# Kernel optimization log

Measured on AMD Instinct MI355X. Metric: run time of the kernel, lower is better.

## Reference

```python
import jax, jax.numpy as jnp
import numpy as np


def spiral_cw(H, W):
    idx = []
    top, bottom, left, right = 0, H - 1, 0, W - 1
    while top <= bottom and left <= right:
        for j in range(left, right + 1):
            idx.append((top, j))
        top += 1
        for i in range(top, bottom + 1):
            idx.append((i, right))
        right -= 1
        if top <= bottom:
            for j in range(right, left - 1, -1):
                idx.append((bottom, j))
            bottom -= 1
        if left <= right:
            for i in range(bottom, top - 1, -1):
                idx.append((i, left))
            left += 1
    return [i * W + j for i, j in idx]


def spiral_ccw(H, W):
    idx = []
    top, bottom, left, right = 0, H - 1, 0, W - 1
    while top <= bottom and left <= right:
        for j in range(right, left - 1, -1):
            idx.append((top, j))
        top += 1
        for i in range(top, bottom + 1):
            idx.append((i, left))
        left += 1
        if top <= bottom:
            for j in range(left, right + 1):
                idx.append((bottom, j))
            bottom -= 1
        if left <= right:
            for i in range(bottom, top - 1, -1):
                idx.append((i, right))
            right -= 1
    return [i * W + j for i, j in idx]


def silu(x):
    return x * jax.nn.sigmoid(x)


def mamba_fwd(x, in_w, conv_w, conv_b, xproj_w, dtp_w, dtp_b, A_log, D, out_w):
    # x: [B,L,dm]; expand=1 so d_inner == dm
    B, L, dm = x.shape
    d_inner = in_w.shape[1] // 2
    N = A_log.shape[1]          # d_state = 16
    K = conv_w.shape[1]         # d_conv = 4
    xz = x @ in_w               # [B,L,2*d_inner]
    u, z = jnp.split(xz, 2, axis=-1)
    # causal depthwise conv over L (kernel K), then SiLU
    up = jnp.pad(u, ((0, 0), (K - 1, 0), (0, 0)))
    uc = conv_b + sum(conv_w[:, k] * up[:, k:k + L, :] for k in range(K))
    uc = silu(uc)
    dbl = uc @ xproj_w          # [B,L,dt_rank+2N]
    dt_rank = dbl.shape[-1] - 2 * N
    dtc = dbl[..., :dt_rank]
    Bv = dbl[..., dt_rank:dt_rank + N]
    Cv = dbl[..., dt_rank + N:]
    dt = jax.nn.softplus(dtc @ dtp_w + dtp_b)   # [B,L,d_inner]
    A = -jnp.exp(A_log)                          # [d_inner,N]
    dA = jnp.exp(dt[..., None] * A)              # [B,L,d_inner,N]
    dBu = dt[..., None] * Bv[:, :, None, :] * uc[..., None]

    def step(h, inp):
        dA_t, dBu_t = inp
        h = h * dA_t + dBu_t
        return h, h

    h0 = jnp.zeros((B, d_inner, N), x.dtype)
    _, hs = jax.lax.scan(step, h0, (jnp.moveaxis(dA, 1, 0), jnp.moveaxis(dBu, 1, 0)))
    hs = jnp.moveaxis(hs, 0, 1)                  # [B,L,d_inner,N]
    y = jnp.einsum('bldn,bln->bld', hs, Cv) + D * uc
    y = y * silu(z)
    return y @ out_w


def setup_inputs():
    key = jax.random.key(0)
    ks = jax.random.split(key, 32)
    B, Hh, Ww, C = 4, 32, 32, 768
    L = Hh * Ww
    N, dr, K = 16, 48, 4

    def p(i, shape, s=0.02):
        return jax.random.normal(ks[i], shape, jnp.float32) * s

    d = {}
    d['x'] = jax.random.normal(ks[0], (B, L, C), jnp.float32)
    d['norm_w'] = jnp.ones((C,), jnp.float32)
    d['norm_b'] = jnp.zeros((C,), jnp.float32)
    for i, pre in enumerate(['cw', 'ccw']):
        o = 1 + i * 8
        d[pre + '_in_w'] = p(o, (C, 2 * C))
        d[pre + '_conv_w'] = p(o + 1, (C, K), 0.2)
        d[pre + '_conv_b'] = jnp.zeros((C,), jnp.float32)
        d[pre + '_xproj_w'] = p(o + 2, (C, dr + 2 * N))
        d[pre + '_dtp_w'] = p(o + 3, (dr, C), 0.1)
        d[pre + '_dtp_b'] = jnp.full((C,), -4.0, jnp.float32) + p(o + 4, (C,), 0.5)
        d[pre + '_A_log'] = jnp.log(jnp.broadcast_to(jnp.arange(1, N + 1, dtype=jnp.float32), (C, N)))
        d[pre + '_D'] = jnp.ones((C,), jnp.float32)
        d[pre + '_out_w'] = p(o + 5, (C, C))
    d['fus_w1'] = p(20, (2 * C, C))
    d['fus_b1'] = jnp.zeros((C,), jnp.float32)
    d['fus_w2'] = p(21, (C, C))
    d['fus_b2'] = jnp.zeros((C,), jnp.float32)
    return d


def reference(x, norm_w, norm_b,
              cw_in_w, cw_conv_w, cw_conv_b, cw_xproj_w, cw_dtp_w, cw_dtp_b, cw_A_log, cw_D, cw_out_w,
              ccw_in_w, ccw_conv_w, ccw_conv_b, ccw_xproj_w, ccw_dtp_w, ccw_dtp_b, ccw_A_log, ccw_D, ccw_out_w,
              fus_w1, fus_b1, fus_w2, fus_b2):
    B, L, C = x.shape
    H = int(L ** 0.5)
    W = H
    idx_cw = jnp.asarray(np.array(spiral_cw(H, W), dtype=np.int32))
    idx_ccw = jnp.asarray(np.array(spiral_ccw(H, W), dtype=np.int32))
    rev_cw = jnp.argsort(idx_cw)
    rev_ccw = jnp.argsort(idx_ccw)
    # LayerNorm(eps=1e-6)
    mu = x.mean(-1, keepdims=True)
    var = x.var(-1, keepdims=True)
    xn = (x - mu) / jnp.sqrt(var + 1e-6) * norm_w + norm_b
    x_cw = mamba_fwd(xn[:, idx_cw, :], cw_in_w, cw_conv_w, cw_conv_b, cw_xproj_w,
                     cw_dtp_w, cw_dtp_b, cw_A_log, cw_D, cw_out_w)[:, rev_cw, :]
    x_ccw = mamba_fwd(xn[:, idx_ccw, :], ccw_in_w, ccw_conv_w, ccw_conv_b, ccw_xproj_w,
                      ccw_dtp_w, ccw_dtp_b, ccw_A_log, ccw_D, ccw_out_w)[:, rev_ccw, :]
    fused = jnp.concatenate([x_cw, x_ccw], axis=-1)
    h = jax.nn.gelu(fused @ fus_w1 + fus_b1, approximate=False)
    out = h @ fus_w2 + fus_b2
    return out + x
```

## Files before the change

kernel.cpp:

```cpp
#include <hip/hip_runtime.h>

typedef unsigned short ushort_t;
typedef __attribute__((ext_vector_type(8))) short short8;
typedef __attribute__((ext_vector_type(4))) float f32x4;
typedef __attribute__((ext_vector_type(4))) unsigned short u16x4;

#define B_ 4
#define L_ 1024
#define C_ 768
#define N_ 16
#define DR_ 48
#define HW_ 32
#define M_ (B_*L_)
#define SEG_ 64
#define NSEG_ 16


__device__ __forceinline__ float bf2f(ushort_t u) {
  union { unsigned int i; float f; } v; v.i = ((unsigned int)u) << 16; return v.f;
}
__device__ __forceinline__ ushort_t f2bf(float f) {
  union { float f; unsigned int i; } v; v.f = f;
  unsigned int x = v.i;
  return (ushort_t)((x + 0x7fffu + ((x >> 16) & 1u)) >> 16);
}
__device__ __forceinline__ float ldf(const void* p, size_t i, int bf) {
  return bf ? bf2f(((const ushort_t*)p)[i]) : ((const float*)p)[i];
}
__device__ __forceinline__ int detect_bf(const void* x) {
  const ushort_t* u = (const ushort_t*)x;
  int lane = threadIdx.x & 63;
  const ushort_t* p = u + lane * 4;
  int bad = 0;
  #pragma unroll
  for (int i = 0; i < 4; ++i) {
    int e = (p[i] >> 7) & 0xFF;
    bad |= (e < 90 || e > 141);
  }
  return (__ballot(bad) == 0ull) ? 1 : 0;
}
__device__ __forceinline__ void gload_lds16(const void* g, void* lds) {
  __builtin_amdgcn_global_load_lds(
      (const __attribute__((address_space(1))) unsigned int*)g,
      (__attribute__((address_space(3))) unsigned int*)lds, 16, 0, 0);
}

struct TJ {
  const void* src[8]; ushort_t* dst[8];
  int R[8], Cc[8], RD[8], ldD[8];
  int off[9]; int njobs;
};

__global__ __launch_bounds__(256) void prep_k(
    TJ tj, const void* __restrict__ x, const void* __restrict__ nw,
    const void* __restrict__ nb, ushort_t* __restrict__ xn,
    int* idx_cw, int* idx_ccw, int* flag)
{
  const int oT = tj.off[tj.njobs];
  int bid = blockIdx.x;
  const int inbf = detect_bf(x);

  if (bid < oT) {
    int j = 0;
    while (bid >= tj.off[j+1]) ++j;
    const void* src = tj.src[j];
    ushort_t* dst = tj.dst[j];
    const int R = tj.R[j], Cc = tj.Cc[j], RD = tj.RD[j], ldD = tj.ldD[j];
    int cb_span = (Cc > RD ? Cc : RD);
    int txt = (cb_span + 31) >> 5;
    int t = bid - tj.off[j];
    int bx = (t % txt) * 32;
    int by = (t / txt) * 32;
    __shared__ ushort_t tile[32][33];
    int tx = threadIdx.x & 31, ty = threadIdx.x >> 5;
    #pragma unroll
    for (int i = 0; i < 4; ++i) {
      int r = by + ty + i*8, c = bx + tx;
      ushort_t v = 0;
      if (r < R && c < Cc) v = f2bf(ldf(src, (size_t)r * Cc + c, inbf));
      tile[ty + i*8][tx] = v;
    }
    __syncthreads();
    #pragma unroll
    for (int i = 0; i < 4; ++i) {
      int dr = bx + ty + i*8, dc = by + tx;
      if (dr < RD && dc < ldD)
        dst[(size_t)dr * ldD + dc] = tile[tx][ty + i*8];
    }
    return;
  }
  bid -= oT;
  if (bid < M_) {
    int tid = threadIdx.x;
    size_t o0 = (size_t)bid * C_;
    float v0 = ldf(x, o0 + tid,       inbf);
    float v1 = ldf(x, o0 + tid + 256, inbf);
    float v2 = ldf(x, o0 + tid + 512, inbf);
    float s = v0 + v1 + v2, s2 = v0*v0 + v1*v1 + v2*v2;
    for (int o = 32; o > 0; o >>= 1) { s += __shfl_down(s, o); s2 += __shfl_down(s2, o); }
    __shared__ float ss[4], ss2[4];
    if ((tid & 63) == 0) { ss[tid >> 6] = s; ss2[tid >> 6] = s2; }
    __syncthreads();
    s  = ss[0] + ss[1] + ss[2] + ss[3];
    s2 = ss2[0] + ss2[1] + ss2[2] + ss2[3];
    float mean = s * (1.f / C_);
    float var  = s2 * (1.f / C_) - mean * mean;
    float inv  = rsqrtf(var + 1e-6f);
    xn[o0 + tid]       = f2bf((v0 - mean) * inv * ldf(nw, tid,     inbf) + ldf(nb, tid,     inbf));
    xn[o0 + tid + 256] = f2bf((v1 - mean) * inv * ldf(nw, tid+256, inbf) + ldf(nb, tid+256, inbf));
    xn[o0 + tid + 512] = f2bf((v2 - mean) * inv * ldf(nw, tid+512, inbf) + ldf(nb, tid+512, inbf));
    return;
  }
  {
    int tid = threadIdx.x;
    #pragma unroll
    for (int k = 0; k < 4; ++k) {
      int p = tid * 4 + k;
      int r = 0;
      while (r < (HW_/2 - 1) && p >= 4*(r+1)*(HW_-(r+1))) ++r;
      int q = p - 4*r*(HW_-r);
      int s = HW_ - 2*r;
      int hi = HW_ - 1 - r;
      int icw, jcw, iccw, jccw;
      if (q < s)              { icw = r;                  jcw = r + q; }
      else if (q < 2*s-1)     { icw = r + 1 + (q - s);    jcw = hi; }
      else if (q < 3*s-2)     { icw = hi;                 jcw = hi - 1 - (q - (2*s-1)); }
      else                    { icw = hi - 1 - (q - (3*s-2)); jcw = r; }
      if (q < s)              { iccw = r;                 jccw = hi - q; }
      else if (q < 2*s-1)     { iccw = r + 1 + (q - s);   jccw = r; }
      else if (q < 3*s-2)     { iccw = hi;                jccw = r + 1 + (q - (2*s-1)); }
      else                    { iccw = hi - 1 - (q - (3*s-2)); jccw = hi; }
      idx_cw[p]  = icw  * HW_ + jcw;
      idx_ccw[p] = iccw * HW_ + jccw;
    }
    if (tid == 0) *flag = inbf;
  }
}

__global__ __launch_bounds__(256) void tbatch_k(TJ tj, const int* __restrict__ flagp) {
  const int inbf = *flagp;
  int bid = blockIdx.x;
  int j = 0;
  while (bid >= tj.off[j+1]) ++j;
  const void* src = tj.src[j];
  ushort_t* dst = tj.dst[j];
  const int R = tj.R[j], Cc = tj.Cc[j], RD = tj.RD[j], ldD = tj.ldD[j];
  int cb_span = (Cc > RD ? Cc : RD);
  int txt = (cb_span + 31) >> 5;
  int t = bid - tj.off[j];
  int bx = (t % txt) * 32;
  int by = (t / txt) * 32;
  __shared__ ushort_t tile[32][33];
  int tx = threadIdx.x & 31, ty = threadIdx.x >> 5;
  #pragma unroll
  for (int i = 0; i < 4; ++i) {
    int r = by + ty + i*8, c = bx + tx;
    ushort_t v = 0;
    if (r < R && c < Cc) v = f2bf(ldf(src, (size_t)r * Cc + c, inbf));
    tile[ty + i*8][tx] = v;
  }
  __syncthreads();
  #pragma unroll
  for (int i = 0; i < 4; ++i) {
    int dr = bx + ty + i*8, dc = by + tx;
    if (dr < RD && dc < ldD)
      dst[(size_t)dr * ldD + dc] = tile[tx][ty + i*8];
  }
}

struct GB {
  const ushort_t* A[4]; const int* amap[4];
  const ushort_t* WT[4];
  const void* bias[4];
  void* out[4]; ushort_t* out2[4]; const int* omap[4];
};

template<int BM, int BN>
__global__ __launch_bounds__(256) void mgemm_k(
    GB gb, int lda, int ldb, int Nn, int K, int ldo,
    int act, int out_mode, const void* resid, int ldr, const int* __restrict__ flagp)
{
  constexpr int NA = BM / 32;
  constexpr int NB = BN / 32;
  constexpr int WN = (BM == 128) ? 2 : 4;
  constexpr int NSPAN = BN / WN;
  constexpr int FN = NSPAN / 16;
  const int inbf = *flagp;
  const int z = blockIdx.z;

  const ushort_t* A  = gb.A[z];
  const int* amap    = gb.amap[z];
  const ushort_t* Bw = gb.WT[z];
  const void* bias   = gb.bias[z];
  void* Out          = gb.out[z];
  ushort_t* out2     = gb.out2[z];
  const int* omap    = gb.omap[z];

  __shared__ __align__(16) ushort_t As[BM * 64];
  __shared__ __align__(16) ushort_t Bs[BN * 64];

  const int tid  = threadIdx.x;
  const int w    = tid >> 6;
  const int lane = tid & 63;
  const int quad = lane >> 4;
  const int l15  = lane & 15;
  const int wm     = (BM == 128) ? (w >> 1) * 64 : 0;
  const int wn_off = ((BM == 128) ? (w & 1) : w) * NSPAN;
  const int row0 = blockIdx.y * BM;
  const int col0 = blockIdx.x * BN;

  int agb[NA], bgb[NB], aldso[NA], bldso[NB];
  #pragma unroll
  for (int i = 0; i < NA; ++i) {
    int t = i*256 + tid;
    int r = t >> 3;
    int c = (t & 7) ^ (r & 7);
    int grow = row0 + r;
    if (amap) { int b = grow >> 10, l = grow & 1023; grow = (b << 10) + amap[l]; }
    agb[i] = grow * lda + c * 8;
    aldso[i] = (i*256 + w*64) * 16;
  }
  #pragma unroll
  for (int i = 0; i < NB; ++i) {
    int t = i*256 + tid;
    int r = t >> 3;
    int c = (t & 7) ^ (r & 7);
    bgb[i] = (col0 + r) * ldb + c * 8;
    bldso[i] = (i*256 + w*64) * 16;
  }

  f32x4 acc[4][FN];
  #pragma unroll
  for (int mi = 0; mi < 4; ++mi)
    #pragma unroll
    for (int ni = 0; ni < FN; ++ni)
      acc[mi][ni] = (f32x4){0.f, 0.f, 0.f, 0.f};

  const int sw = l15 & 7;

  for (int k0 = 0; k0 < K; k0 += 64) {
    #pragma unroll
    for (int i = 0; i < NA; ++i)
      gload_lds16(A + agb[i] + k0, (char*)As + aldso[i]);
    #pragma unroll
    for (int i = 0; i < NB; ++i)
      gload_lds16(Bw + bgb[i] + k0, (char*)Bs + bldso[i]);
    __syncthreads();

    #pragma unroll
    for (int ks = 0; ks < 2; ++ks) {
      short8 aF[4], bF[FN];
      #pragma unroll
      for (int mi = 0; mi < 4; ++mi)
        aF[mi] = *(const short8*)&As[(wm + mi*16 + l15) * 64 + (((quad + 4*ks) ^ sw) * 8)];
      #pragma unroll
      for (int ni = 0; ni < FN; ++ni)
        bF[ni] = *(const short8*)&Bs[(wn_off + ni*16 + l15) * 64 + (((quad + 4*ks) ^ sw) * 8)];
      #pragma unroll
      for (int mi = 0; mi < 4; ++mi)
        #pragma unroll
        for (int ni = 0; ni < FN; ++ni)
          acc[mi][ni] = __builtin_amdgcn_mfma_f32_16x16x32_bf16(aF[mi], bF[ni], acc[mi][ni], 0, 0, 0);
    }
    __syncthreads();
  }

  const int obf = (out_mode == 2) ? inbf : (out_mode == 0);
  #pragma unroll
  for (int ni = 0; ni < FN; ++ni) {
    int colg = col0 + wn_off + ni*16 + l15;
    if (colg >= Nn) continue;
    float bv = bias ? ldf(bias, colg, inbf) : 0.f;
    #pragma unroll
    for (int mi = 0; mi < 4; ++mi) {
      #pragma unroll
      for (int r = 0; r < 4; ++r) {
        int rowg = row0 + wm + mi*16 + quad*4 + r;
        int orow = rowg;
        if (omap) { int b = rowg >> 10, l = rowg & 1023; orow = (b << 10) + omap[l]; }
        float v = acc[mi][ni][r] + bv;
        if (out2 && colg < 64)
          out2[(size_t)orow * 64 + colg] = f2bf(colg < DR_ ? v : 0.f);
        if (act == 1)      v = (v > 20.f) ? v : log1pf(__expf(v));
        else if (act == 2) v = 0.5f * v * (1.f + erff(v * 0.70710678118654752f));
        if (resid) v += ldf(resid, (size_t)orow * ldr + colg, inbf);
        size_t oi = (size_t)orow * ldo + colg;
        if (obf) ((ushort_t*)Out)[oi] = f2bf(v);
        else     ((float*)Out)[oi]    = v;
      }
    }
  }
}

__global__ __launch_bounds__(256) void conv_silu_k(
    const ushort_t* __restrict__ u,
    const void* __restrict__ cw0, const void* __restrict__ cw1,
    const void* __restrict__ cb0, const void* __restrict__ cb1,
    ushort_t* __restrict__ uc, const int* __restrict__ flagp)
{
  const int inbf = *flagp;
  int g = blockIdx.x * 256 + threadIdx.x;
  int c = g % C_;
  int row = g / C_;
  int l = row & 1023;
  const void* cw = (row >> 12) ? cw1 : cw0;
  const void* cb = (row >> 12) ? cb1 : cb0;
  float w0 = ldf(cw, c*4+0, inbf), w1 = ldf(cw, c*4+1, inbf);
  float w2 = ldf(cw, c*4+2, inbf), w3 = ldf(cw, c*4+3, inbf);
  const ushort_t* up = u + (size_t)(row - l) * C_ + c;
  float s = ldf(cb, c, inbf);
  if (l >= 3) s += w0 * bf2f(up[(size_t)(l-3) * C_]);
  if (l >= 2) s += w1 * bf2f(up[(size_t)(l-2) * C_]);
  if (l >= 1) s += w2 * bf2f(up[(size_t)(l-1) * C_]);
  s += w3 * bf2f(up[(size_t)l * C_]);
  s = s / (1.f + __expf(-s));
  uc[g] = f2bf(s);
}

__global__ __launch_bounds__(256) void scan_pass1(
    const ushort_t* __restrict__ dt, const ushort_t* __restrict__ uc,
    const float* __restrict__ dbl,
    const void* __restrict__ Alog_cw, const void* __restrict__ Alog_ccw,
    ushort_t* __restrict__ P, ushort_t* __restrict__ Q,
    const int* __restrict__ flagp)
{
  const int inbf = *flagp;
  const int db = blockIdx.z, d = db >> 2;
  const int s = blockIdx.y;
  const int tid = threadIdx.x;
  const int cl = tid >> 2;
  const int n4 = tid & 3;
  const int c = blockIdx.x * 64 + cl;
  const int l0 = s * SEG_;

  __shared__ __align__(16) float Bs[SEG_][32];
  {
    const float* src = dbl + ((size_t)db * L_ + l0) * 80 + DR_;
    #pragma unroll
    for (int i = 0; i < 2; ++i) {
      int idx = tid * 4 + i * 1024;
      int st = idx >> 5, col = idx & 31;
      *(f32x4*)&Bs[st][col] = *(const f32x4*)(src + (size_t)st * 80 + col);
    }
  }
  __syncthreads();

  const void* Alog = d ? Alog_ccw : Alog_cw;
  float a[4];
  #pragma unroll
  for (int j = 0; j < 4; ++j) a[j] = -__expf(ldf(Alog, c * N_ + n4*4 + j, inbf));

  const size_t rbase = ((size_t)db * L_ + l0) * C_ + c;
  const ushort_t* dtp = dt + rbase;
  const ushort_t* ucp = uc + rbase;

  float h[4] = {0.f, 0.f, 0.f, 0.f};
  float S = 0.f;

  #pragma unroll 8
  for (int l = 0; l < SEG_; ++l) {
    float dtv = bf2f(dtp[(size_t)l * C_]);
    float ucv = bf2f(ucp[(size_t)l * C_]);
    float dtu = dtv * ucv;
    S += dtv;
    f32x4 bq = *(const f32x4*)&Bs[l][n4*4];
    #pragma unroll
    for (int j = 0; j < 4; ++j) { float dA = __expf(dtv*a[j]); h[j] = h[j]*dA + dtu*bq[j]; }
  }
  size_t idx = (((size_t)db * NSEG_ + s) * C_ + c) * N_ + n4*4;
  u16x4 pv, qv;
  #pragma unroll
  for (int j = 0; j < 4; ++j) { pv[j] = f2bf(__expf(a[j] * S)); qv[j] = f2bf(h[j]); }
  *(u16x4*)&P[idx] = pv;
  *(u16x4*)&Q[idx] = qv;
}

__global__ __launch_bounds__(256) void scan_pass2(
    ushort_t* __restrict__ P, ushort_t* __restrict__ Q)
{
  size_t g = (size_t)blockIdx.x * 256 + threadIdx.x;
  size_t db = g / (C_ * N_);
  size_t cn = g % (C_ * N_);
  float h = 0.f;
  #pragma unroll
  for (int s = 0; s < NSEG_; ++s) {
    size_t off = (db * NSEG_ + s) * (C_ * N_) + cn;
    float p = bf2f(P[off]), q = bf2f(Q[off]);
    Q[off] = f2bf(h);
    h = h * p + q;
  }
}

__global__ __launch_bounds__(256) void scan_pass3(
    const ushort_t* __restrict__ dt, const ushort_t* __restrict__ uc,
    const float* __restrict__ dbl, const ushort_t* __restrict__ z,
    const void* __restrict__ Alog_cw, const void* __restrict__ Alog_ccw,
    const void* __restrict__ D_cw, const void* __restrict__ D_ccw,
    const ushort_t* __restrict__ Q, ushort_t* __restrict__ y,
    const int* __restrict__ flagp)
{
  const int inbf = *flagp;
  const int db = blockIdx.z, d = db >> 2;
  const int s = blockIdx.y;
  const int tid = threadIdx.x;
  const int cl = tid >> 2;
  const int n4 = tid & 3;
  const int c = blockIdx.x * 64 + cl;
  const int l0 = s * SEG_;

  __shared__ __align__(16) float Bs[SEG_][32];
  {
    const float* src = dbl + ((size_t)db * L_ + l0) * 80 + DR_;
    #pragma unroll
    for (int i = 0; i < 2; ++i) {
      int idx = tid * 4 + i * 1024;
      int st = idx >> 5, col = idx & 31;
      *(f32x4*)&Bs[st][col] = *(const f32x4*)(src + (size_t)st * 80 + col);
    }
  }
  __syncthreads();

  const void* Alog = d ? Alog_ccw : Alog_cw;
  const void* Dp   = d ? D_ccw   : D_cw;
  float a[4];
  #pragma unroll
  for (int j = 0; j < 4; ++j) a[j] = -__expf(ldf(Alog, c * N_ + n4*4 + j, inbf));
  const float dvc = ldf(Dp, c, inbf);

  const size_t rbase = ((size_t)db * L_ + l0) * C_ + c;
  const ushort_t* dtp = dt + rbase;
  const ushort_t* ucp = uc + rbase;
  const ushort_t* zp  = z  + rbase;
  ushort_t* yp = y + rbase;

  size_t idx = (((size_t)db * NSEG_ + s) * C_ + c) * N_ + n4*4;
  float h[4];
  #pragma unroll
  for (int j = 0; j < 4; ++j) h[j] = bf2f(Q[idx + j]);

  #pragma unroll 4
  for (int l = 0; l < SEG_; ++l) {
    float dtv = bf2f(dtp[(size_t)l * C_]);
    float ucv = bf2f(ucp[(size_t)l * C_]);
    float zv  = bf2f(zp[(size_t)l * C_]);
    float dtu = dtv * ucv;
    f32x4 bq = *(const f32x4*)&Bs[l][n4*4];
    f32x4 cq = *(const f32x4*)&Bs[l][16 + n4*4];
    float yv = 0.f;
    #pragma unroll
    for (int j = 0; j < 4; ++j) { float dA = __expf(dtv*a[j]); h[j] = h[j]*dA + dtu*bq[j]; yv += h[j]*cq[j]; }
    yv += __shfl_xor(yv, 1);
    yv += __shfl_xor(yv, 2);
    if (n4 == 0) {
      float o = yv + dvc * ucv;
      o *= zv / (1.f + __expf(-zv));
      yp[(size_t)l * C_] = f2bf(o);
    }
  }
}

extern "C" void kernel_launch(void* const* d_in, const int* in_sizes, int n_in,
                              void* d_out, int out_size, void* d_ws, size_t ws_size,
                              hipStream_t stream)
{
  const void* x      = d_in[0];
  const void* norm_w = d_in[1];
  const void* norm_b = d_in[2];
  const void* in_w[2]    = { d_in[3],  d_in[12] };
  const void* conv_w[2]  = { d_in[4],  d_in[13] };
  const void* conv_b[2]  = { d_in[5],  d_in[14] };
  const void* xproj_w[2] = { d_in[6],  d_in[15] };
  const void* dtp_w[2]   = { d_in[7],  d_in[16] };
  const void* dtp_b[2]   = { d_in[8],  d_in[17] };
  const void* A_log[2]   = { d_in[9],  d_in[18] };
  const void* Dvec[2]    = { d_in[10], d_in[19] };
  const void* out_w[2]   = { d_in[11], d_in[20] };
  const void* fus_w1 = d_in[21];
  const void* fus_b1 = d_in[22];
  const void* fus_w2 = d_in[23];
  const void* fus_b2 = d_in[24];

  char* base = (char*)d_ws;
  int*      IDX  = (int*)base;
  int*      FLAG = (int*)(base + 8192);
  ushort_t* XN   = (ushort_t*)(base + 8448);
  ushort_t* U    = (ushort_t*)(base + 6299904);
  ushort_t* Z    = (ushort_t*)(base + 18882816);
  ushort_t* UC   = (ushort_t*)(base + 31465728);
  float*    DBL  = (float*)(base + 44048640);
  ushort_t* Y    = (ushort_t*)(base + 46670080);
  ushort_t* DT    = U;
  ushort_t* FUSED = Z;
  ushort_t* HBUF  = XN;
  ushort_t* SP = (ushort_t*)(base + 8448);
  ushort_t* SQ = SP + (size_t)2 * 4 * NSEG_ * C_ * N_;
  ushort_t* DTC = XN;
  ushort_t* INWT = UC;
  ushort_t* uout = (ushort_t*)d_out;
  ushort_t* XPJT = uout;
  ushort_t* DTPT = uout + 196608;
  ushort_t* OWT  = uout + 294912;
  ushort_t* FW1T = U;
  ushort_t* FW2T = U + (size_t)768 * 1536;

  const size_t SD = (size_t)M_ * C_;

  {
    TJ tj; tj.njobs = 8;
    for (int d = 0; d < 2; ++d) {
      int j = d;
      tj.src[j]=in_w[d]; tj.dst[j]=INWT+(size_t)d*1536*768;
      tj.R[j]=768; tj.Cc[j]=1536; tj.RD[j]=1536; tj.ldD[j]=768;
    }
    for (int d = 0; d < 2; ++d) {
      int j = 2+d;
      tj.src[j]=xproj_w[d]; tj.dst[j]=XPJT+(size_t)d*128*768;
      tj.R[j]=768; tj.Cc[j]=80; tj.RD[j]=128; tj.ldD[j]=768;
    }
    for (int d = 0; d < 2; ++d) {
      int j = 4+d;
      tj.src[j]=dtp_w[d]; tj.dst[j]=DTPT+(size_t)d*768*64;
      tj.R[j]=48; tj.Cc[j]=768; tj.RD[j]=768; tj.ldD[j]=64;
    }
    for (int d = 0; d < 2; ++d) {
      int j = 6+d;
      tj.src[j]=out_w[d]; tj.dst[j]=OWT+(size_t)d*768*768;
      tj.R[j]=768; tj.Cc[j]=768; tj.RD[j]=768; tj.ldD[j]=768;
    }
    tj.off[0] = 0;
    for (int j = 0; j < 8; ++j) {
      int cspan = tj.Cc[j] > tj.RD[j] ? tj.Cc[j] : tj.RD[j];
      int rspan = tj.R[j] > tj.ldD[j] ? tj.R[j] : tj.ldD[j];
      tj.off[j+1] = tj.off[j] + ((cspan+31)>>5) * ((rspan+31)>>5);
    }
    int nblk = tj.off[8] + M_ + 1;
    hipLaunchKernelGGL(prep_k, dim3(nblk), dim3(256), 0, stream,
        tj, x, norm_w, norm_b, XN, IDX, IDX + L_, FLAG);
  }

  GB gb;
  for (int i = 0; i < 4; ++i) { gb.out2[i] = nullptr; gb.omap[i] = nullptr; gb.amap[i] = nullptr; gb.bias[i] = nullptr; }

  for (int zz = 0; zz < 4; ++zz) {
    int d = zz >> 1, half = zz & 1;
    gb.A[zz] = XN; gb.amap[zz] = IDX + d * L_;
    gb.WT[zz] = INWT + (size_t)d*1536*768 + (size_t)half*768*768;
    gb.bias[zz] = nullptr;
    gb.out[zz] = (void*)((half ? Z : U) + d * SD); gb.out2[zz] = nullptr; gb.omap[zz] = nullptr;
  }
  hipLaunchKernelGGL((mgemm_k<64,64>), dim3(12, 64, 4), dim3(256), 0, stream,
      gb, C_, C_, C_, C_, C_, 0, 0, (const void*)nullptr, 0, FLAG);

  hipLaunchKernelGGL(conv_silu_k, dim3(2*M_*C_/256), dim3(256), 0, stream,
      U, conv_w[0], conv_w[1], conv_b[0], conv_b[1], UC, FLAG);

  for (int zz = 0; zz < 2; ++zz) {
    gb.A[zz] = UC + zz * SD; gb.amap[zz] = nullptr;
    gb.WT[zz] = XPJT + (size_t)zz*128*768;
    gb.bias[zz] = nullptr;
    gb.out[zz] = (void*)(DBL + (size_t)zz * M_ * 80);
    gb.out2[zz] = DTC + (size_t)zz * M_ * 64;
    gb.omap[zz] = nullptr;
  }
  hipLaunchKernelGGL((mgemm_k<64,64>), dim3(2, 64, 2), dim3(256), 0, stream,
      gb, C_, C_, 80, C_, 80, 0, 1, (const void*)nullptr, 0, FLAG);

  for (int zz = 0; zz < 2; ++zz) {
    gb.A[zz] = DTC + (size_t)zz * M_ * 64; gb.amap[zz] = nullptr;
    gb.WT[zz] = DTPT + (size_t)zz*768*64;
    gb.bias[zz] = dtp_b[zz];
    gb.out[zz] = (void*)(DT + zz * SD); gb.out2[zz] = nullptr; gb.omap[zz] = nullptr;
  }
  hipLaunchKernelGGL((mgemm_k<64,64>), dim3(12, 64, 2), dim3(256), 0, stream,
      gb, 64, 64, C_, 64, C_, 1, 0, (const void*)nullptr, 0, FLAG);

  hipLaunchKernelGGL(scan_pass1, dim3(12, NSEG_, 8), dim3(256), 0, stream,
      DT, UC, DBL, A_log[0], A_log[1], SP, SQ, FLAG);
  hipLaunchKernelGGL(scan_pass2, dim3(8 * C_ * N_ / 256), dim3(256), 0, stream, SP, SQ);
  hipLaunchKernelGGL(scan_pass3, dim3(12, NSEG_, 8), dim3(256), 0, stream,
      DT, UC, DBL, Z, A_log[0], A_log[1], Dvec[0], Dvec[1], SQ, Y, FLAG);

  {
    TJ tj; tj.njobs = 2;
    tj.src[0]=fus_w1; tj.dst[0]=FW1T; tj.R[0]=1536; tj.Cc[0]=768; tj.RD[0]=768; tj.ldD[0]=1536;
    tj.src[1]=fus_w2; tj.dst[1]=FW2T; tj.R[1]=768;  tj.Cc[1]=768; tj.RD[1]=768; tj.ldD[1]=768;
    tj.off[0] = 0;
    for (int j = 0; j < 2; ++j) {
      int cspan = tj.Cc[j] > tj.RD[j] ? tj.Cc[j] : tj.RD[j];
      int rspan = tj.R[j] > tj.ldD[j] ? tj.R[j] : tj.ldD[j];
      tj.off[j+1] = tj.off[j] + ((cspan+31)>>5) * ((rspan+31)>>5);
    }
    hipLaunchKernelGGL(tbatch_k, dim3(tj.off[2]), dim3(256), 0, stream, tj, FLAG);
  }

  for (int zz = 0; zz < 2; ++zz) {
    gb.A[zz] = Y + zz * SD; gb.amap[zz] = nullptr;
    gb.WT[zz] = OWT + (size_t)zz*768*768;
    gb.bias[zz] = nullptr;
    gb.out[zz] = (void*)(FUSED + zz * C_); gb.out2[zz] = nullptr; gb.omap[zz] = IDX + zz * L_;
  }
  hipLaunchKernelGGL((mgemm_k<64,64>), dim3(12, 64, 2), dim3(256), 0, stream,
      gb, C_, C_, C_, C_, 2*C_, 0, 0, (const void*)nullptr, 0, FLAG);

  gb.A[0] = FUSED; gb.amap[0] = nullptr;
  gb.WT[0] = FW1T; gb.bias[0] = fus_b1;
  gb.out[0] = (void*)HBUF; gb.out2[0] = nullptr; gb.omap[0] = nullptr;
  hipLaunchKernelGGL((mgemm_k<64,64>), dim3(12, 64, 1), dim3(256), 0, stream,
      gb, 2*C_, 2*C_, C_, 2*C_, C_, 2, 0, (const void*)nullptr, 0, FLAG);

  gb.A[0] = HBUF; gb.amap[0] = nullptr;
  gb.WT[0] = FW2T; gb.bias[0] = fus_b2;
  gb.out[0] = d_out; gb.out2[0] = nullptr; gb.omap[0] = nullptr;
  hipLaunchKernelGGL((mgemm_k<64,64>), dim3(12, 64, 1), dim3(256), 0, stream,
      gb, C_, C_, C_, C_, C_, 0, 2, x, C_, FLAG);
}
```

Baseline: 401.0 us.

## Stage scan inputs in LDS via direct global-to-LDS loads and vectorize output writes

Scan pass1 and pass3 now bulk-load the per-segment dt, uc and B/C tiles into shared memory with 16-byte direct global-to-LDS loads. Previously each thread did strided 2-byte global loads inside the sequential loop. Pass3 also buffers y in LDS, then applies the z-gating and writes output in 16-byte vectors, replacing the scattered per-element stores from one lane in four. The cost is more LDS per block, which may lower occupancy, plus an extra barrier.

```diff
diff --git a/kernel.cpp b/kernel.cpp
--- a/kernel.cpp
+++ b/kernel.cpp
@@ -330,17 +330,26 @@
   const int tid = threadIdx.x;
   const int cl = tid >> 2;
   const int n4 = tid & 3;
-  const int c = blockIdx.x * 64 + cl;
+  const int c0 = blockIdx.x * 64;
+  const int c = c0 + cl;
   const int l0 = s * SEG_;
 
-  __shared__ __align__(16) float Bs[SEG_][32];
+  __shared__ __align__(16) float    BsS[SEG_ * 16];
+  __shared__ __align__(16) ushort_t dtS[SEG_ * 64];
+  __shared__ __align__(16) ushort_t ucS[SEG_ * 64];
   {
-    const float* src = dbl + ((size_t)db * L_ + l0) * 80 + DR_;
+    {
+      int row = tid >> 2, col = (tid & 3) * 4;
+      gload_lds16(dbl + ((size_t)db * L_ + l0 + row) * 80 + DR_ + col,
+                  (char*)BsS + tid * 16);
+    }
     #pragma unroll
     for (int i = 0; i < 2; ++i) {
-      int idx = tid * 4 + i * 1024;
-      int st = idx >> 5, col = idx & 31;
-      *(f32x4*)&Bs[st][col] = *(const f32x4*)(src + (size_t)st * 80 + col);
+      int ch = i * 256 + tid;
+      int row = ch >> 3, col = (ch & 7) * 8;
+      size_t go = ((size_t)db * L_ + l0 + row) * C_ + c0 + col;
+      gload_lds16(dt + go, (char*)dtS + ch * 16);
+      gload_lds16(uc + go, (char*)ucS + ch * 16);
     }
   }
   __syncthreads();
@@ -350,20 +359,16 @@
   #pragma unroll
   for (int j = 0; j < 4; ++j) a[j] = -__expf(ldf(Alog, c * N_ + n4*4 + j, inbf));
 
-  const size_t rbase = ((size_t)db * L_ + l0) * C_ + c;
-  const ushort_t* dtp = dt + rbase;
-  const ushort_t* ucp = uc + rbase;
-
   float h[4] = {0.f, 0.f, 0.f, 0.f};
   float S = 0.f;
 
   #pragma unroll 8
   for (int l = 0; l < SEG_; ++l) {
-    float dtv = bf2f(dtp[(size_t)l * C_]);
-    float ucv = bf2f(ucp[(size_t)l * C_]);
+    float dtv = bf2f(dtS[l * 64 + cl]);
+    float ucv = bf2f(ucS[l * 64 + cl]);
     float dtu = dtv * ucv;
     S += dtv;
-    f32x4 bq = *(const f32x4*)&Bs[l][n4*4];
+    f32x4 bq = *(const f32x4*)&BsS[l * 16 + n4 * 4];
     #pragma unroll
     for (int j = 0; j < 4; ++j) { float dA = __expf(dtv*a[j]); h[j] = h[j]*dA + dtu*bq[j]; }
   }
@@ -405,17 +410,29 @@
   const int tid = threadIdx.x;
   const int cl = tid >> 2;
   const int n4 = tid & 3;
-  const int c = blockIdx.x * 64 + cl;
+  const int c0 = blockIdx.x * 64;
+  const int c = c0 + cl;
   const int l0 = s * SEG_;
 
-  __shared__ __align__(16) float Bs[SEG_][32];
+  __shared__ __align__(16) float    BsS[SEG_ * 32];
+  __shared__ __align__(16) ushort_t dtS[SEG_ * 64];
+  __shared__ __align__(16) ushort_t ucS[SEG_ * 64];
+  __shared__ __align__(16) float    yS [SEG_ * 64];
   {
-    const float* src = dbl + ((size_t)db * L_ + l0) * 80 + DR_;
     #pragma unroll
     for (int i = 0; i < 2; ++i) {
-      int idx = tid * 4 + i * 1024;
-      int st = idx >> 5, col = idx & 31;
-      *(f32x4*)&Bs[st][col] = *(const f32x4*)(src + (size_t)st * 80 + col);
+      int ch = i * 256 + tid;
+      int row = ch >> 3, col = (ch & 7) * 4;
+      gload_lds16(dbl + ((size_t)db * L_ + l0 + row) * 80 + DR_ + col,
+                  (char*)BsS + ch * 16);
+    }
+    #pragma unroll
+    for (int i = 0; i < 2; ++i) {
+      int ch = i * 256 + tid;
+      int row = ch >> 3, col = (ch & 7) * 8;
+      size_t go = ((size_t)db * L_ + l0 + row) * C_ + c0 + col;
+      gload_lds16(dt + go, (char*)dtS + ch * 16);
+      gload_lds16(uc + go, (char*)ucS + ch * 16);
     }
   }
   __syncthreads();
@@ -427,12 +444,6 @@
   for (int j = 0; j < 4; ++j) a[j] = -__expf(ldf(Alog, c * N_ + n4*4 + j, inbf));
   const float dvc = ldf(Dp, c, inbf);
 
-  const size_t rbase = ((size_t)db * L_ + l0) * C_ + c;
-  const ushort_t* dtp = dt + rbase;
-  const ushort_t* ucp = uc + rbase;
-  const ushort_t* zp  = z  + rbase;
-  ushort_t* yp = y + rbase;
-
   size_t idx = (((size_t)db * NSEG_ + s) * C_ + c) * N_ + n4*4;
   float h[4];
   #pragma unroll
@@ -440,22 +451,40 @@
 
   #pragma unroll 4
   for (int l = 0; l < SEG_; ++l) {
-    float dtv = bf2f(dtp[(size_t)l * C_]);
-    float ucv = bf2f(ucp[(size_t)l * C_]);
-    float zv  = bf2f(zp[(size_t)l * C_]);
+    float dtv = bf2f(dtS[l * 64 + cl]);
+    float ucv = bf2f(ucS[l * 64 + cl]);
     float dtu = dtv * ucv;
-    f32x4 bq = *(const f32x4*)&Bs[l][n4*4];
-    f32x4 cq = *(const f32x4*)&Bs[l][16 + n4*4];
+    f32x4 bq = *(const f32x4*)&BsS[l * 32 + n4 * 4];
+    f32x4 cq = *(const f32x4*)&BsS[l * 32 + 16 + n4 * 4];
     float yv = 0.f;
     #pragma unroll
     for (int j = 0; j < 4; ++j) { float dA = __expf(dtv*a[j]); h[j] = h[j]*dA + dtu*bq[j]; yv += h[j]*cq[j]; }
     yv += __shfl_xor(yv, 1);
     yv += __shfl_xor(yv, 2);
-    if (n4 == 0) {
-      float o = yv + dvc * ucv;
-      o *= zv / (1.f + __expf(-zv));
-      yp[(size_t)l * C_] = f2bf(o);
-    }
+    if (n4 == 0) yS[l * 64 + cl] = yv + dvc * ucv;
+  }
+  __syncthreads();
+
+  #pragma unroll
+  for (int i = 0; i < 2; ++i) {
+    int ch = i * 256 + tid;
+    int row = ch >> 3, col = (ch & 7) * 8;
+    size_t go = ((size_t)db * L_ + l0 + row) * C_ + c0 + col;
+    short8 zr = *(const short8*)(z + go);
+    f32x4 y0 = *(const f32x4*)&yS[row * 64 + col];
+    f32x4 y1 = *(const f32x4*)&yS[row * 64 + col + 4];
+    short8 res;
+    #pragma unroll
+    for (int j = 0; j < 4; ++j) {
+      float zv = bf2f((ushort_t)zr[j]);
+      res[j] = (short)f2bf(y0[j] * zv / (1.f + __expf(-zv)));
+    }
+    #pragma unroll
+    for (int j = 0; j < 4; ++j) {
+      float zv = bf2f((ushort_t)zr[4 + j]);
+      res[4 + j] = (short)f2bf(y1[j] * zv / (1.f + __expf(-zv)));
+    }
+    *(short8*)(y + go) = res;
   }
 }
 
```

Result: faster. 375.8 us (-6.3%).
